# Kernel optimization log

Hardware: AMD Instinct MI355X
Metric: run time of the kernel (lower is better)

The kernel has to match this reference:

```python
import jax, jax.numpy as jnp
import numpy as np

N_NODES = 50000
N_EDGES = 800000
N_RELS = 65
D = 64
N_GRAPHS = 512


def setup_inputs() -> dict:
    key = jax.random.key(0)
    ks = jax.random.split(key, 20)
    inp = {
        "node_feats": jax.random.normal(ks[0], (N_NODES, D), dtype=jnp.float32),
        "etypes": jax.random.randint(ks[1], (N_EDGES,), 0, N_RELS),
        "src": jax.random.randint(ks[2], (N_EDGES,), 0, N_NODES),
        "dst": jax.random.randint(ks[3], (N_EDGES,), 0, N_NODES),
        "graph_ids": jnp.sort(jax.random.randint(ks[4], (N_NODES,), 0, N_GRAPHS)),
    }
    s = 1.0 / np.sqrt(D)
    # 3 RGCN layers: per-relation weights (basis with num_bases=num_rels == full) + bias
    for i, k in zip(range(1, 4), (ks[5], ks[6], ks[7])):
        inp[f"W_rel{i}"] = jax.random.normal(k, (N_RELS, D, D), dtype=jnp.float32) * s
        inp[f"b{i}"] = jnp.zeros((D,), dtype=jnp.float32)
    # 3 FC layers
    for i, k in zip(range(1, 4), (ks[8], ks[9], ks[10])):
        inp[f"fc_W{i}"] = jax.random.normal(k, (D, D), dtype=jnp.float32) * s
        inp[f"fc_b{i}"] = jnp.zeros((D,), dtype=jnp.float32)
    inp["pred_W"] = jax.random.normal(ks[11], (D, 2), dtype=jnp.float32) * s
    inp["pred_b"] = jnp.zeros((2,), dtype=jnp.float32)
    return inp


def _rgcn_layer(h, W, b, etypes, src, dst):
    # all-relation projection: [N, R, K]
    proj = jnp.einsum('nd,rdk->nrk', h, W)
    # per-edge gather of relation-specific message: [E, K]
    msg = proj[src, etypes]
    # scatter-sum into destination nodes
    agg = jax.ops.segment_sum(msg, dst, num_segments=h.shape[0])
    return jax.nn.relu(agg + b)


def reference(node_feats, etypes, src, dst, graph_ids,
              W_rel1, b1, W_rel2, b2, W_rel3, b3,
              fc_W1, fc_b1, fc_W2, fc_b2, fc_W3, fc_b3,
              pred_W, pred_b):
    h = node_feats
    h = _rgcn_layer(h, W_rel1, b1, etypes, src, dst)
    h = _rgcn_layer(h, W_rel2, b2, etypes, src, dst)
    h = _rgcn_layer(h, W_rel3, b3, etypes, src, dst)
    # sum-pool nodes per graph: [G, D]
    g = jax.ops.segment_sum(h, graph_ids, num_segments=N_GRAPHS)
    g = jax.nn.relu(g @ fc_W1 + fc_b1)
    g = jax.nn.relu(g @ fc_W2 + fc_b2)
    g = jax.nn.relu(g @ fc_W3 + fc_b3)
    return g @ pred_W + pred_b
```

## Files before the change

kernel.cpp:

```cpp
#include <hip/hip_runtime.h>
#include <hip/hip_bf16.h>

#define N_NODES 50000
#define N_EDGES 800000
#define N_RELS 65
#define DIM 64
#define N_GRAPHS 512

#define SORT_BLOCKS 256
#define CHUNK ((N_EDGES + SORT_BLOCKS - 1) / SORT_BLOCKS)

#define SCAN_BLK 512
#define NSCAN_BLKS ((N_NODES + SCAN_BLK - 1) / SCAN_BLK)

#define MSG_BLOCKS 1024
#define NWAVES (MSG_BLOCKS * 4)

typedef __attribute__((ext_vector_type(8))) short short8;
typedef __attribute__((ext_vector_type(4))) float f32x4;


__global__ void conv_h_zero_kernel(const float* __restrict__ x, __hip_bfloat16* __restrict__ y,
                                   int* __restrict__ cnt_d, int* __restrict__ cnt_g) {
    int i = blockIdx.x * 256 + threadIdx.x;
    if (i < N_NODES * DIM) y[i] = __float2bfloat16(x[i]);
    if (i < N_NODES) cnt_d[i] = 0;
    if (i < N_GRAPHS) cnt_g[i] = 0;
}

__global__ void conv_wt3_kernel(const float* __restrict__ W1, const float* __restrict__ W2,
                                const float* __restrict__ W3,
                                __hip_bfloat16* __restrict__ Wt1,
                                __hip_bfloat16* __restrict__ Wt2,
                                __hip_bfloat16* __restrict__ Wt3) {
    const int n = N_RELS * DIM * DIM;
    int i = blockIdx.x * 256 + threadIdx.x;
    if (i >= 3 * n) return;
    int which = i / n, j = i - which * n;
    const float* W = (which == 0) ? W1 : (which == 1) ? W2 : W3;
    __hip_bfloat16* Wt = (which == 0) ? Wt1 : (which == 1) ? Wt2 : Wt3;
    int r = j >> 12, rest = j & 4095;
    int nn = rest >> 6, k = rest & 63;
    Wt[(size_t)r * 4096 + nn * 64 + k] = __float2bfloat16(W[(size_t)r * 4096 + k * 64 + nn]);
}


__global__ __launch_bounds__(256) void hist2_kernel(const int* __restrict__ et,
                                                    int* __restrict__ blk_hist) {
    __shared__ int lh[N_RELS];
    int t = threadIdx.x, b = blockIdx.x;
    if (t < N_RELS) lh[t] = 0;
    __syncthreads();
    int lo = b * CHUNK;
    int hi = lo + CHUNK; if (hi > N_EDGES) hi = N_EDGES;
    for (int i = lo + t; i < hi; i += 256) atomicAdd(&lh[et[i]], 1);
    __syncthreads();
    if (t < N_RELS) blk_hist[b * N_RELS + t] = lh[t];
}

__global__ __launch_bounds__(256) void relwave_kernel(const int* __restrict__ blk_hist,
                                                      int* __restrict__ blk_off,
                                                      int* __restrict__ rel_tot) {
    int wave = blockIdx.x * 4 + (threadIdx.x >> 6);
    int lane = threadIdx.x & 63;
    if (wave >= N_RELS) return;
    int run = 0;
    for (int c = 0; c < SORT_BLOCKS; c += 64) {
        int b = c + lane;
        int v = blk_hist[b * N_RELS + wave];
        int x = v;
        #pragma unroll
        for (int off = 1; off < 64; off <<= 1) {
            int y = __shfl_up(x, off);
            if (lane >= off) x += y;
        }
        blk_off[b * N_RELS + wave] = run + x - v;
        run += __shfl(x, 63);
    }
    if (lane == 0) rel_tot[wave] = run;
}

__global__ __launch_bounds__(128) void relbase_kernel(const int* __restrict__ rel_tot,
                                                      int* __restrict__ rel_ptr,
                                                      int* __restrict__ tile_base) {
    __shared__ int tot[N_RELS];
    int t = threadIdx.x;
    if (t < N_RELS) tot[t] = rel_tot[t];
    __syncthreads();
    if (t == 0) {
        int s = 0, tt = 0;
        for (int q = 0; q < N_RELS; ++q) {
            rel_ptr[q] = s; s += tot[q];
            tile_base[q] = tt; tt += (tot[q] + 15) >> 4;
        }
        rel_ptr[N_RELS] = N_EDGES;
        tile_base[N_RELS] = tt;
    }
}

__global__ __launch_bounds__(256) void scatter2_kernel(
    const int* __restrict__ et, const int* __restrict__ src,
    const int* __restrict__ dst, const int* __restrict__ blk_off,
    const int* __restrict__ rel_ptr,
    int* __restrict__ src_s, int* __restrict__ dst_s) {
    __shared__ int cur[N_RELS];
    int t = threadIdx.x, b = blockIdx.x;
    if (t < N_RELS) cur[t] = blk_off[b * N_RELS + t] + rel_ptr[t];
    __syncthreads();
    int lo = b * CHUNK;
    int hi = lo + CHUNK; if (hi > N_EDGES) hi = N_EDGES;
    for (int i = lo + t; i < hi; i += 256) {
        int r = et[i];
        int p = atomicAdd(&cur[r], 1);
        src_s[p] = src[i];
        dst_s[p] = dst[i];
    }
}


__global__ void histdst_kernel(const int* __restrict__ dst, int* __restrict__ cnt_d) {
    int i = blockIdx.x * 256 + threadIdx.x;
    if (i < N_EDGES) atomicAdd(&cnt_d[dst[i]], 1);
}

__global__ __launch_bounds__(SCAN_BLK) void scanblk_kernel(const int* __restrict__ cnt,
                                                           int* __restrict__ outv,
                                                           int* __restrict__ blk_tot) {
    __shared__ int tmp[SCAN_BLK];
    int t = threadIdx.x;
    int i = blockIdx.x * SCAN_BLK + t;
    int v = (i < N_NODES) ? cnt[i] : 0;
    tmp[t] = v;
    __syncthreads();
    for (int off = 1; off < SCAN_BLK; off <<= 1) {
        int add = (t >= off) ? tmp[t - off] : 0;
        __syncthreads();
        tmp[t] += add;
        __syncthreads();
    }
    if (i < N_NODES) outv[i] = tmp[t] - v;
    if (t == SCAN_BLK - 1) blk_tot[blockIdx.x] = tmp[t];
}

__global__ void scantop_kernel(int* __restrict__ blk_tot, int* __restrict__ blk_base) {
    if (threadIdx.x == 0 && blockIdx.x == 0) {
        int run = 0;
        for (int b = 0; b < NSCAN_BLKS; ++b) { blk_base[b] = run; run += blk_tot[b]; }
    }
}

__global__ __launch_bounds__(SCAN_BLK) void scanadd_kernel(int* __restrict__ outv,
                                                           int* __restrict__ cursor,
                                                           const int* __restrict__ blk_base) {
    int i = blockIdx.x * SCAN_BLK + threadIdx.x;
    if (i < N_NODES) {
        int v = outv[i] + blk_base[blockIdx.x];
        outv[i] = v;
        cursor[i] = v;
    }
}

__global__ void dpos_kernel(const int* __restrict__ dst_s, int* __restrict__ cursor,
                            int* __restrict__ dpos) {
    int i = blockIdx.x * 256 + threadIdx.x;
    if (i < N_EDGES) dpos[i] = atomicAdd(&cursor[dst_s[i]], 1);
}


__global__ void histgid_kernel(const int* __restrict__ gid, int* __restrict__ cnt_g) {
    int i = blockIdx.x * 256 + threadIdx.x;
    if (i < N_NODES) atomicAdd(&cnt_g[gid[i]], 1);
}

__global__ __launch_bounds__(512) void scangid_kernel(const int* __restrict__ cnt_g,
                                                      int* __restrict__ g_ptr) {
    __shared__ int tmp[512];
    int t = threadIdx.x;
    int v = (t < N_GRAPHS) ? cnt_g[t] : 0;
    tmp[t] = v;
    __syncthreads();
    for (int off = 1; off < 512; off <<= 1) {
        int add = (t >= off) ? tmp[t - off] : 0;
        __syncthreads();
        tmp[t] += add;
        __syncthreads();
    }
    if (t < N_GRAPHS) g_ptr[t] = tmp[t] - v;
}


__global__ __launch_bounds__(256) void msg_mfma_kernel(
    const __hip_bfloat16* __restrict__ hb, const __hip_bfloat16* __restrict__ Wt,
    const int* __restrict__ rel_ptr, const int* __restrict__ tile_base,
    const int* __restrict__ src_s, const int* __restrict__ dpos,
    __hip_bfloat16* __restrict__ msg) {
    __shared__ __align__(16) unsigned short stA[4][16 * 72];
    __shared__ __align__(16) float stC[4][16 * 68];

    int t = threadIdx.x;
    int w = t >> 6, lane = t & 63;
    int quad = lane >> 4, m16 = lane & 15;
    int wave = blockIdx.x * 4 + w;

    int ntiles = tile_base[N_RELS];
    int tpw = (ntiles + NWAVES - 1) / NWAVES;
    int T = wave * tpw;
    int T1 = T + tpw; if (T1 > ntiles) T1 = ntiles;
    if (T >= T1) return;

    unsigned short* sa = &stA[w][0];
    float* sc = &stC[w][0];

    int r = 0;
    while (T >= tile_base[r + 1]) ++r;

    while (T < T1) {
        int chunk_end = tile_base[r + 1]; if (chunk_end > T1) chunk_end = T1;
        int e_base = rel_ptr[r], t_base = tile_base[r];
        int seg_end = rel_ptr[r + 1];

        const __hip_bfloat16* Wr = Wt + (size_t)r * (DIM * DIM);
        short8 bf00 = *(const short8*)(Wr + (0 * 16 + m16) * DIM + 0 * 32 + quad * 8);
        short8 bf01 = *(const short8*)(Wr + (1 * 16 + m16) * DIM + 0 * 32 + quad * 8);
        short8 bf02 = *(const short8*)(Wr + (2 * 16 + m16) * DIM + 0 * 32 + quad * 8);
        short8 bf03 = *(const short8*)(Wr + (3 * 16 + m16) * DIM + 0 * 32 + quad * 8);
        short8 bf10 = *(const short8*)(Wr + (0 * 16 + m16) * DIM + 1 * 32 + quad * 8);
        short8 bf11 = *(const short8*)(Wr + (1 * 16 + m16) * DIM + 1 * 32 + quad * 8);
        short8 bf12 = *(const short8*)(Wr + (2 * 16 + m16) * DIM + 1 * 32 + quad * 8);
        short8 bf13 = *(const short8*)(Wr + (3 * 16 + m16) * DIM + 1 * 32 + quad * 8);

        auto eidx = [&](int TT) {
            int i = e_base + (TT - t_base) * 16 + lane;
            return i < N_EDGES ? i : N_EDGES - 1;
        };

        int sv_c, dp_c, sv_n = 0, dp_n = 0, sv_nn = 0, dp_nn = 0;
        uint4 g0_c, g1_c;
        {
            int i0 = eidx(T);
            sv_c = src_s[i0]; dp_c = dpos[i0];
            int r0 = lane >> 3;
            int s0 = __shfl(sv_c, r0);
            int s1 = __shfl(sv_c, r0 + 8);
            g0_c = *(const uint4*)(hb + (size_t)s0 * DIM + (lane & 7) * 8);
            g1_c = *(const uint4*)(hb + (size_t)s1 * DIM + (lane & 7) * 8);
            if (T + 1 < chunk_end) {
                int i1 = eidx(T + 1);
                sv_n = src_s[i1]; dp_n = dpos[i1];
            }
        }

        for (; T < chunk_end; ++T) {
            int e0 = e_base + (T - t_base) * 16;
            int rows = seg_end - e0; if (rows > 16) rows = 16;

            int r0 = lane >> 3;
            *(uint4*)&sa[r0 * 72 + (lane & 7) * 8] = g0_c;
            *(uint4*)&sa[(r0 + 8) * 72 + (lane & 7) * 8] = g1_c;

            uint4 g0_n, g1_n;
            bool hasN = (T + 1 < chunk_end);
            if (hasN) {
                int s0 = __shfl(sv_n, r0);
                int s1 = __shfl(sv_n, r0 + 8);
                g0_n = *(const uint4*)(hb + (size_t)s0 * DIM + (lane & 7) * 8);
                g1_n = *(const uint4*)(hb + (size_t)s1 * DIM + (lane & 7) * 8);
            }
            if (T + 2 < chunk_end) {
                int i2 = eidx(T + 2);
                sv_nn = src_s[i2]; dp_nn = dpos[i2];
            }

            short8 a0 = *(const short8*)&sa[m16 * 72 + quad * 8];
            short8 a1 = *(const short8*)&sa[m16 * 72 + 32 + quad * 8];

            f32x4 c0 = {0.f, 0.f, 0.f, 0.f}, c1 = c0, c2 = c0, c3 = c0;
            c0 = __builtin_amdgcn_mfma_f32_16x16x32_bf16(a0, bf00, c0, 0, 0, 0);
            c1 = __builtin_amdgcn_mfma_f32_16x16x32_bf16(a0, bf01, c1, 0, 0, 0);
            c2 = __builtin_amdgcn_mfma_f32_16x16x32_bf16(a0, bf02, c2, 0, 0, 0);
            c3 = __builtin_amdgcn_mfma_f32_16x16x32_bf16(a0, bf03, c3, 0, 0, 0);
            c0 = __builtin_amdgcn_mfma_f32_16x16x32_bf16(a1, bf10, c0, 0, 0, 0);
            c1 = __builtin_amdgcn_mfma_f32_16x16x32_bf16(a1, bf11, c1, 0, 0, 0);
            c2 = __builtin_amdgcn_mfma_f32_16x16x32_bf16(a1, bf12, c2, 0, 0, 0);
            c3 = __builtin_amdgcn_mfma_f32_16x16x32_bf16(a1, bf13, c3, 0, 0, 0);

            #pragma unroll
            for (int reg = 0; reg < 4; ++reg) {
                int rr = (quad * 4 + reg) * 68 + m16;
                sc[rr +  0] = c0[reg];
                sc[rr + 16] = c1[reg];
                sc[rr + 32] = c2[reg];
                sc[rr + 48] = c3[reg];
            }

            int orow = lane >> 2;
            if (orow < rows) {
                int c0i = (lane & 3) * 16;
                float vs[16];
                *(f32x4*)&vs[0]  = *(const f32x4*)&sc[orow * 68 + c0i + 0];
                *(f32x4*)&vs[4]  = *(const f32x4*)&sc[orow * 68 + c0i + 4];
                *(f32x4*)&vs[8]  = *(const f32x4*)&sc[orow * 68 + c0i + 8];
                *(f32x4*)&vs[12] = *(const f32x4*)&sc[orow * 68 + c0i + 12];
                unsigned short us[16];
                #pragma unroll
                for (int i = 0; i < 16; ++i)
                    us[i] = __hip_bfloat16_raw(__float2bfloat16(vs[i])).x;
                int dprow = __shfl(dp_c, orow);
                __hip_bfloat16* dst = msg + (size_t)dprow * DIM + c0i;
                *(uint4*)dst = *(const uint4*)&us[0];
                *(uint4*)(dst + 8) = *(const uint4*)&us[8];
            }

            if (hasN) { g0_c = g0_n; g1_c = g1_n; }
            sv_c = sv_n; dp_c = dp_n;
            sv_n = sv_nn; dp_n = dp_nn;
        }
        ++r;
        while (T < T1 && T >= tile_base[r + 1]) ++r;
    }
}


__global__ __launch_bounds__(256) void agg_kernel(
    const __hip_bfloat16* __restrict__ msg, const int* __restrict__ row_ptr,
    const int* __restrict__ cnt_d, const float* __restrict__ b,
    __hip_bfloat16* __restrict__ hout) {
    int wave = blockIdx.x * 4 + (threadIdx.x >> 6);
    int lane = threadIdx.x & 63;
    if (wave >= N_NODES) return;
    int j0 = row_ptr[wave];
    int n  = cnt_d[wave];
    int rgrp = lane >> 3, dgrp = lane & 7;

    float a[8] = {0.f, 0.f, 0.f, 0.f, 0.f, 0.f, 0.f, 0.f};
    for (int jj = 0; jj < n; jj += 8) {
        int row = jj + rgrp;
        if (row < n) {
            uint4 d = *(const uint4*)(msg + (size_t)(j0 + row) * DIM + dgrp * 8);
            a[0] += __uint_as_float(d.x << 16);
            a[1] += __uint_as_float(d.x & 0xffff0000u);
            a[2] += __uint_as_float(d.y << 16);
            a[3] += __uint_as_float(d.y & 0xffff0000u);
            a[4] += __uint_as_float(d.z << 16);
            a[5] += __uint_as_float(d.z & 0xffff0000u);
            a[6] += __uint_as_float(d.w << 16);
            a[7] += __uint_as_float(d.w & 0xffff0000u);
        }
    }
    #pragma unroll
    for (int i = 0; i < 8; ++i) {
        a[i] += __shfl_xor(a[i], 8);
        a[i] += __shfl_xor(a[i], 16);
        a[i] += __shfl_xor(a[i], 32);
    }
    if (rgrp == 0) {
        unsigned short us[8];
        #pragma unroll
        for (int i = 0; i < 8; ++i) {
            float v = a[i] + b[dgrp * 8 + i];
            us[i] = __hip_bfloat16_raw(__float2bfloat16(v > 0.f ? v : 0.f)).x;
        }
        *(uint4*)(hout + (size_t)wave * DIM + dgrp * 8) = *(const uint4*)us;
    }
}


__global__ __launch_bounds__(256) void poolfc_kernel(
    const __hip_bfloat16* __restrict__ h, const int* __restrict__ g_ptr,
    const int* __restrict__ cnt_g,
    const float* __restrict__ W1, const float* __restrict__ b1,
    const float* __restrict__ W2, const float* __restrict__ b2,
    const float* __restrict__ W3, const float* __restrict__ b3,
    const float* __restrict__ pW, const float* __restrict__ pb,
    float* __restrict__ out) {
    int wave = blockIdx.x * 4 + (threadIdx.x >> 6);
    int lane = threadIdx.x & 63;
    if (wave >= N_GRAPHS) return;
    int j0 = g_ptr[wave];
    int n  = cnt_g[wave];
    int rgrp = lane >> 3, dgrp = lane & 7;

    float a[8] = {0.f, 0.f, 0.f, 0.f, 0.f, 0.f, 0.f, 0.f};
    for (int jj = 0; jj < n; jj += 8) {
        int row = jj + rgrp;
        if (row < n) {
            uint4 d = *(const uint4*)(h + (size_t)(j0 + row) * DIM + dgrp * 8);
            a[0] += __uint_as_float(d.x << 16);
            a[1] += __uint_as_float(d.x & 0xffff0000u);
            a[2] += __uint_as_float(d.y << 16);
            a[3] += __uint_as_float(d.y & 0xffff0000u);
            a[4] += __uint_as_float(d.z << 16);
            a[5] += __uint_as_float(d.z & 0xffff0000u);
            a[6] += __uint_as_float(d.w << 16);
            a[7] += __uint_as_float(d.w & 0xffff0000u);
        }
    }
    #pragma unroll
    for (int i = 0; i < 8; ++i) {
        a[i] += __shfl_xor(a[i], 8);
        a[i] += __shfl_xor(a[i], 16);
        a[i] += __shfl_xor(a[i], 32);
    }
    float v;
    {
        float acc = b1[lane];
        #pragma unroll
        for (int o = 0; o < 8; ++o)
            #pragma unroll
            for (int q = 0; q < 8; ++q)
                acc += __shfl(a[o], q) * W1[(q * 8 + o) * DIM + lane];
        v = acc > 0.f ? acc : 0.f;
    }
    {
        float acc = b2[lane];
        #pragma unroll
        for (int d = 0; d < DIM; ++d)
            acc += __shfl(v, d) * W2[d * DIM + lane];
        v = acc > 0.f ? acc : 0.f;
    }
    {
        float acc = b3[lane];
        #pragma unroll
        for (int d = 0; d < DIM; ++d)
            acc += __shfl(v, d) * W3[d * DIM + lane];
        v = acc > 0.f ? acc : 0.f;
    }
    float p0 = v * pW[lane * 2 + 0];
    float p1 = v * pW[lane * 2 + 1];
    #pragma unroll
    for (int off = 32; off > 0; off >>= 1) {
        p0 += __shfl_down(p0, off);
        p1 += __shfl_down(p1, off);
    }
    if (lane == 0) {
        out[wave * 2 + 0] = p0 + pb[0];
        out[wave * 2 + 1] = p1 + pb[1];
    }
}


extern "C" void kernel_launch(void* const* d_in, const int* in_sizes, int n_in,
                              void* d_out, int out_size, void* d_ws, size_t ws_size,
                              hipStream_t stream) {
    const float* node_feats = (const float*)d_in[0];
    const int*   etypes     = (const int*)d_in[1];
    const int*   src        = (const int*)d_in[2];
    const int*   dst        = (const int*)d_in[3];
    const int*   graph_ids  = (const int*)d_in[4];
    const float* W1 = (const float*)d_in[5];
    const float* b1 = (const float*)d_in[6];
    const float* W2 = (const float*)d_in[7];
    const float* b2 = (const float*)d_in[8];
    const float* W3 = (const float*)d_in[9];
    const float* b3 = (const float*)d_in[10];
    const float* fcW1 = (const float*)d_in[11];
    const float* fcb1 = (const float*)d_in[12];
    const float* fcW2 = (const float*)d_in[13];
    const float* fcb2 = (const float*)d_in[14];
    const float* fcW3 = (const float*)d_in[15];
    const float* fcb3 = (const float*)d_in[16];
    const float* pW = (const float*)d_in[17];
    const float* pb = (const float*)d_in[18];
    float* out = (float*)d_out;

    char* p = (char*)d_ws;
    auto alloc = [&](size_t bytes) -> void* {
        void* r = (void*)p;
        p += (bytes + 255) & ~(size_t)255;
        return r;
    };
    int* blk_hist  = (int*)alloc((size_t)SORT_BLOCKS * N_RELS * sizeof(int));
    int* blk_off   = (int*)alloc((size_t)SORT_BLOCKS * N_RELS * sizeof(int));
    int* rel_tot   = (int*)alloc(N_RELS * sizeof(int));
    int* rel_ptr   = (int*)alloc((N_RELS + 1) * sizeof(int));
    int* tile_base = (int*)alloc((N_RELS + 1) * sizeof(int));
    int* src_s     = (int*)alloc((size_t)N_EDGES * sizeof(int));
    int* dst_s     = (int*)alloc((size_t)N_EDGES * sizeof(int));
    int* dpos      = (int*)alloc((size_t)N_EDGES * sizeof(int));
    int* cnt_d     = (int*)alloc((size_t)N_NODES * sizeof(int));
    int* row_ptr   = (int*)alloc((size_t)N_NODES * sizeof(int));
    int* cursor_d  = (int*)alloc((size_t)N_NODES * sizeof(int));
    int* blk_tot   = (int*)alloc(NSCAN_BLKS * sizeof(int));
    int* blk_base  = (int*)alloc(NSCAN_BLKS * sizeof(int));
    int* cnt_g     = (int*)alloc(N_GRAPHS * sizeof(int));
    int* g_ptr     = (int*)alloc(N_GRAPHS * sizeof(int));
    __hip_bfloat16* hb0 = (__hip_bfloat16*)alloc((size_t)N_NODES * DIM * sizeof(__hip_bfloat16));
    __hip_bfloat16* hb1 = (__hip_bfloat16*)alloc((size_t)N_NODES * DIM * sizeof(__hip_bfloat16));
    __hip_bfloat16* Wt1 = (__hip_bfloat16*)alloc((size_t)N_RELS * DIM * DIM * sizeof(__hip_bfloat16));
    __hip_bfloat16* Wt2 = (__hip_bfloat16*)alloc((size_t)N_RELS * DIM * DIM * sizeof(__hip_bfloat16));
    __hip_bfloat16* Wt3 = (__hip_bfloat16*)alloc((size_t)N_RELS * DIM * DIM * sizeof(__hip_bfloat16));
    __hip_bfloat16* msg = (__hip_bfloat16*)alloc((size_t)N_EDGES * DIM * sizeof(__hip_bfloat16));

    const int EBLK = (N_EDGES + 255) / 256;
    const int HBLK = (N_NODES * DIM + 255) / 256;
    const int W3BLK = (3 * N_RELS * DIM * DIM + 255) / 256;
    const int NBLK256 = (N_NODES + 255) / 256;
    const int AGG_BLOCKS = (N_NODES + 3) / 4;

    conv_h_zero_kernel<<<HBLK, 256, 0, stream>>>(node_feats, hb0, cnt_d, cnt_g);
    conv_wt3_kernel<<<W3BLK, 256, 0, stream>>>(W1, W2, W3, Wt1, Wt2, Wt3);

    hist2_kernel<<<SORT_BLOCKS, 256, 0, stream>>>(etypes, blk_hist);
    relwave_kernel<<<(N_RELS + 3) / 4, 256, 0, stream>>>(blk_hist, blk_off, rel_tot);
    relbase_kernel<<<1, 128, 0, stream>>>(rel_tot, rel_ptr, tile_base);
    scatter2_kernel<<<SORT_BLOCKS, 256, 0, stream>>>(etypes, src, dst, blk_off, rel_ptr,
                                                     src_s, dst_s);

    histdst_kernel<<<EBLK, 256, 0, stream>>>(dst, cnt_d);
    scanblk_kernel<<<NSCAN_BLKS, SCAN_BLK, 0, stream>>>(cnt_d, row_ptr, blk_tot);
    scantop_kernel<<<1, 64, 0, stream>>>(blk_tot, blk_base);
    scanadd_kernel<<<NSCAN_BLKS, SCAN_BLK, 0, stream>>>(row_ptr, cursor_d, blk_base);
    dpos_kernel<<<EBLK, 256, 0, stream>>>(dst_s, cursor_d, dpos);

    histgid_kernel<<<NBLK256, 256, 0, stream>>>(graph_ids, cnt_g);
    scangid_kernel<<<1, 512, 0, stream>>>(cnt_g, g_ptr);

    msg_mfma_kernel<<<MSG_BLOCKS, 256, 0, stream>>>(hb0, Wt1, rel_ptr, tile_base,
                                                    src_s, dpos, msg);
    agg_kernel<<<AGG_BLOCKS, 256, 0, stream>>>(msg, row_ptr, cnt_d, b1, hb1);

    msg_mfma_kernel<<<MSG_BLOCKS, 256, 0, stream>>>(hb1, Wt2, rel_ptr, tile_base,
                                                    src_s, dpos, msg);
    agg_kernel<<<AGG_BLOCKS, 256, 0, stream>>>(msg, row_ptr, cnt_d, b2, hb0);

    msg_mfma_kernel<<<MSG_BLOCKS, 256, 0, stream>>>(hb0, Wt3, rel_ptr, tile_base,
                                                    src_s, dpos, msg);
    agg_kernel<<<AGG_BLOCKS, 256, 0, stream>>>(msg, row_ptr, cnt_d, b3, hb1);

    poolfc_kernel<<<(N_GRAPHS + 3) / 4, 256, 0, stream>>>(hb1, g_ptr, cnt_g,
                                                          fcW1, fcb1, fcW2, fcb2,
                                                          fcW3, fcb3, pW, pb, out);
}
```

Baseline: 421.4 us.

## Merge preprocessing kernels and deepen gather prefetch in message kernel

Folds the weight transpose, destination histogram and graph-id histogram into the relation histogram kernel. Merges the relation scan with the base computation, and the graph-id scan with the top-level scan, which cuts the launch count by about five. The message MFMA kernel now prefetches edge indices three tiles ahead and gathers two tiles ahead to hide gather latency. This raises register pressure, and the merged histogram kernel runs its loops serially over only 256 blocks, so it has less parallelism than the separate launches.

```diff
diff --git a/kernel.cpp b/kernel.cpp
--- a/kernel.cpp
+++ b/kernel.cpp
@@ -28,64 +28,66 @@
     if (i < N_GRAPHS) cnt_g[i] = 0;
 }
 
-__global__ void conv_wt3_kernel(const float* __restrict__ W1, const float* __restrict__ W2,
-                                const float* __restrict__ W3,
-                                __hip_bfloat16* __restrict__ Wt1,
-                                __hip_bfloat16* __restrict__ Wt2,
-                                __hip_bfloat16* __restrict__ Wt3) {
-    const int n = N_RELS * DIM * DIM;
-    int i = blockIdx.x * 256 + threadIdx.x;
-    if (i >= 3 * n) return;
-    int which = i / n, j = i - which * n;
-    const float* W = (which == 0) ? W1 : (which == 1) ? W2 : W3;
-    __hip_bfloat16* Wt = (which == 0) ? Wt1 : (which == 1) ? Wt2 : Wt3;
-    int r = j >> 12, rest = j & 4095;
-    int nn = rest >> 6, k = rest & 63;
-    Wt[(size_t)r * 4096 + nn * 64 + k] = __float2bfloat16(W[(size_t)r * 4096 + k * 64 + nn]);
-}
-
-
-__global__ __launch_bounds__(256) void hist2_kernel(const int* __restrict__ et,
-                                                    int* __restrict__ blk_hist) {
+
+__global__ __launch_bounds__(256) void hist_all_kernel(
+    const int* __restrict__ et, const int* __restrict__ dst,
+    const int* __restrict__ gid, int* __restrict__ blk_hist,
+    int* __restrict__ cnt_d, int* __restrict__ cnt_g,
+    const float* __restrict__ W1, const float* __restrict__ W2,
+    const float* __restrict__ W3,
+    __hip_bfloat16* __restrict__ Wt1, __hip_bfloat16* __restrict__ Wt2,
+    __hip_bfloat16* __restrict__ Wt3) {
     __shared__ int lh[N_RELS];
     int t = threadIdx.x, b = blockIdx.x;
+    int gtid = b * 256 + t;
     if (t < N_RELS) lh[t] = 0;
     __syncthreads();
     int lo = b * CHUNK;
     int hi = lo + CHUNK; if (hi > N_EDGES) hi = N_EDGES;
-    for (int i = lo + t; i < hi; i += 256) atomicAdd(&lh[et[i]], 1);
+    for (int i = lo + t; i < hi; i += 256) {
+        atomicAdd(&lh[et[i]], 1);
+        atomicAdd(&cnt_d[dst[i]], 1);
+    }
+    for (int i = gtid; i < N_NODES; i += SORT_BLOCKS * 256)
+        atomicAdd(&cnt_g[gid[i]], 1);
+    const int WN = N_RELS * DIM * DIM;
+    for (int i = gtid; i < 3 * WN; i += SORT_BLOCKS * 256) {
+        int which = i / WN, j = i - which * WN;
+        const float* W = (which == 0) ? W1 : (which == 1) ? W2 : W3;
+        __hip_bfloat16* Wt = (which == 0) ? Wt1 : (which == 1) ? Wt2 : Wt3;
+        int r = j >> 12, rest = j & 4095;
+        int nn = rest >> 6, k = rest & 63;
+        Wt[(size_t)r * 4096 + nn * 64 + k] =
+            __float2bfloat16(W[(size_t)r * 4096 + k * 64 + nn]);
+    }
     __syncthreads();
     if (t < N_RELS) blk_hist[b * N_RELS + t] = lh[t];
 }
 
-__global__ __launch_bounds__(256) void relwave_kernel(const int* __restrict__ blk_hist,
-                                                      int* __restrict__ blk_off,
-                                                      int* __restrict__ rel_tot) {
-    int wave = blockIdx.x * 4 + (threadIdx.x >> 6);
-    int lane = threadIdx.x & 63;
-    if (wave >= N_RELS) return;
-    int run = 0;
-    for (int c = 0; c < SORT_BLOCKS; c += 64) {
-        int b = c + lane;
-        int v = blk_hist[b * N_RELS + wave];
-        int x = v;
-        #pragma unroll
-        for (int off = 1; off < 64; off <<= 1) {
-            int y = __shfl_up(x, off);
-            if (lane >= off) x += y;
-        }
-        blk_off[b * N_RELS + wave] = run + x - v;
-        run += __shfl(x, 63);
-    }
-    if (lane == 0) rel_tot[wave] = run;
-}
-
-__global__ __launch_bounds__(128) void relbase_kernel(const int* __restrict__ rel_tot,
-                                                      int* __restrict__ rel_ptr,
-                                                      int* __restrict__ tile_base) {
+
+__global__ __launch_bounds__(1024) void relwave2_kernel(const int* __restrict__ blk_hist,
+                                                        int* __restrict__ blk_off,
+                                                        int* __restrict__ rel_ptr,
+                                                        int* __restrict__ tile_base) {
     __shared__ int tot[N_RELS];
     int t = threadIdx.x;
-    if (t < N_RELS) tot[t] = rel_tot[t];
+    int w = t >> 6, lane = t & 63;
+    for (int r = w; r < N_RELS; r += 16) {
+        int run = 0;
+        for (int c = 0; c < SORT_BLOCKS; c += 64) {
+            int b = c + lane;
+            int v = blk_hist[b * N_RELS + r];
+            int x = v;
+            #pragma unroll
+            for (int off = 1; off < 64; off <<= 1) {
+                int y = __shfl_up(x, off);
+                if (lane >= off) x += y;
+            }
+            blk_off[b * N_RELS + r] = run + x - v;
+            run += __shfl(x, 63);
+        }
+        if (lane == 0) tot[r] = run;
+    }
     __syncthreads();
     if (t == 0) {
         int s = 0, tt = 0;
@@ -97,6 +99,7 @@
         tile_base[N_RELS] = tt;
     }
 }
+
 
 __global__ __launch_bounds__(256) void scatter2_kernel(
     const int* __restrict__ et, const int* __restrict__ src,
@@ -118,11 +121,6 @@
 }
 
 
-__global__ void histdst_kernel(const int* __restrict__ dst, int* __restrict__ cnt_d) {
-    int i = blockIdx.x * 256 + threadIdx.x;
-    if (i < N_EDGES) atomicAdd(&cnt_d[dst[i]], 1);
-}
-
 __global__ __launch_bounds__(SCAN_BLK) void scanblk_kernel(const int* __restrict__ cnt,
                                                            int* __restrict__ outv,
                                                            int* __restrict__ blk_tot) {
@@ -142,10 +140,28 @@
     if (t == SCAN_BLK - 1) blk_tot[blockIdx.x] = tmp[t];
 }
 
-__global__ void scantop_kernel(int* __restrict__ blk_tot, int* __restrict__ blk_base) {
-    if (threadIdx.x == 0 && blockIdx.x == 0) {
+__global__ __launch_bounds__(64) void scantop_gid_kernel(
+    const int* __restrict__ blk_tot, int* __restrict__ blk_base,
+    const int* __restrict__ cnt_g, int* __restrict__ g_ptr) {
+    int lane = threadIdx.x;
+    if (blockIdx.x == 0) {
+        if (lane == 0) {
+            int run = 0;
+            for (int b = 0; b < NSCAN_BLKS; ++b) { blk_base[b] = run; run += blk_tot[b]; }
+        }
+    } else {
         int run = 0;
-        for (int b = 0; b < NSCAN_BLKS; ++b) { blk_base[b] = run; run += blk_tot[b]; }
+        for (int c = 0; c < N_GRAPHS; c += 64) {
+            int v = cnt_g[c + lane];
+            int x = v;
+            #pragma unroll
+            for (int off = 1; off < 64; off <<= 1) {
+                int y = __shfl_up(x, off);
+                if (lane >= off) x += y;
+            }
+            g_ptr[c + lane] = run + x - v;
+            run += __shfl(x, 63);
+        }
     }
 }
 
@@ -167,28 +183,6 @@
 }
 
 
-__global__ void histgid_kernel(const int* __restrict__ gid, int* __restrict__ cnt_g) {
-    int i = blockIdx.x * 256 + threadIdx.x;
-    if (i < N_NODES) atomicAdd(&cnt_g[gid[i]], 1);
-}
-
-__global__ __launch_bounds__(512) void scangid_kernel(const int* __restrict__ cnt_g,
-                                                      int* __restrict__ g_ptr) {
-    __shared__ int tmp[512];
-    int t = threadIdx.x;
-    int v = (t < N_GRAPHS) ? cnt_g[t] : 0;
-    tmp[t] = v;
-    __syncthreads();
-    for (int off = 1; off < 512; off <<= 1) {
-        int add = (t >= off) ? tmp[t - off] : 0;
-        __syncthreads();
-        tmp[t] += add;
-        __syncthreads();
-    }
-    if (t < N_GRAPHS) g_ptr[t] = tmp[t] - v;
-}
-
-
 __global__ __launch_bounds__(256) void msg_mfma_kernel(
     const __hip_bfloat16* __restrict__ hb, const __hip_bfloat16* __restrict__ Wt,
     const int* __restrict__ rel_ptr, const int* __restrict__ tile_base,
@@ -210,6 +204,7 @@
 
     unsigned short* sa = &stA[w][0];
     float* sc = &stC[w][0];
+    int r0l = lane >> 3;
 
     int r = 0;
     while (T >= tile_base[r + 1]) ++r;
@@ -220,56 +215,46 @@
         int seg_end = rel_ptr[r + 1];
 
         const __hip_bfloat16* Wr = Wt + (size_t)r * (DIM * DIM);
-        short8 bf00 = *(const short8*)(Wr + (0 * 16 + m16) * DIM + 0 * 32 + quad * 8);
-        short8 bf01 = *(const short8*)(Wr + (1 * 16 + m16) * DIM + 0 * 32 + quad * 8);
-        short8 bf02 = *(const short8*)(Wr + (2 * 16 + m16) * DIM + 0 * 32 + quad * 8);
-        short8 bf03 = *(const short8*)(Wr + (3 * 16 + m16) * DIM + 0 * 32 + quad * 8);
-        short8 bf10 = *(const short8*)(Wr + (0 * 16 + m16) * DIM + 1 * 32 + quad * 8);
-        short8 bf11 = *(const short8*)(Wr + (1 * 16 + m16) * DIM + 1 * 32 + quad * 8);
-        short8 bf12 = *(const short8*)(Wr + (2 * 16 + m16) * DIM + 1 * 32 + quad * 8);
-        short8 bf13 = *(const short8*)(Wr + (3 * 16 + m16) * DIM + 1 * 32 + quad * 8);
-
-        auto eidx = [&](int TT) {
-            int i = e_base + (TT - t_base) * 16 + lane;
-            return i < N_EDGES ? i : N_EDGES - 1;
+        short8 bf00 = *(const short8*)(Wr + (0 * 16 + m16) * DIM + quad * 8);
+        short8 bf01 = *(const short8*)(Wr + (1 * 16 + m16) * DIM + quad * 8);
+        short8 bf02 = *(const short8*)(Wr + (2 * 16 + m16) * DIM + quad * 8);
+        short8 bf03 = *(const short8*)(Wr + (3 * 16 + m16) * DIM + quad * 8);
+        short8 bf10 = *(const short8*)(Wr + (0 * 16 + m16) * DIM + 32 + quad * 8);
+        short8 bf11 = *(const short8*)(Wr + (1 * 16 + m16) * DIM + 32 + quad * 8);
+        short8 bf12 = *(const short8*)(Wr + (2 * 16 + m16) * DIM + 32 + quad * 8);
+        short8 bf13 = *(const short8*)(Wr + (3 * 16 + m16) * DIM + 32 + quad * 8);
+
+        auto loadidx = [&](int TT, int& sv, int& dp) {
+            int TC = TT < chunk_end ? TT : chunk_end - 1;
+            int i = e_base + (TC - t_base) * 16 + lane;
+            if (i >= N_EDGES) i = N_EDGES - 1;
+            sv = src_s[i]; dp = dpos[i];
         };
-
-        int sv_c, dp_c, sv_n = 0, dp_n = 0, sv_nn = 0, dp_nn = 0;
-        uint4 g0_c, g1_c;
-        {
-            int i0 = eidx(T);
-            sv_c = src_s[i0]; dp_c = dpos[i0];
-            int r0 = lane >> 3;
-            int s0 = __shfl(sv_c, r0);
-            int s1 = __shfl(sv_c, r0 + 8);
-            g0_c = *(const uint4*)(hb + (size_t)s0 * DIM + (lane & 7) * 8);
-            g1_c = *(const uint4*)(hb + (size_t)s1 * DIM + (lane & 7) * 8);
-            if (T + 1 < chunk_end) {
-                int i1 = eidx(T + 1);
-                sv_n = src_s[i1]; dp_n = dpos[i1];
-            }
-        }
+        auto gather = [&](int sv, uint4& g0, uint4& g1) {
+            int s0 = __shfl(sv, r0l);
+            int s1 = __shfl(sv, r0l + 8);
+            g0 = *(const uint4*)(hb + (size_t)s0 * DIM + (lane & 7) * 8);
+            g1 = *(const uint4*)(hb + (size_t)s1 * DIM + (lane & 7) * 8);
+        };
+
+        int sv0, dp0, sv1, dp1, sv2, dp2, sv3, dp3;
+        uint4 gc0, gc1, gn0, gn1;
+        loadidx(T,     sv0, dp0);
+        loadidx(T + 1, sv1, dp1);
+        loadidx(T + 2, sv2, dp2);
+        gather(sv0, gc0, gc1);
+        gather(sv1, gn0, gn1);
 
         for (; T < chunk_end; ++T) {
             int e0 = e_base + (T - t_base) * 16;
             int rows = seg_end - e0; if (rows > 16) rows = 16;
 
-            int r0 = lane >> 3;
-            *(uint4*)&sa[r0 * 72 + (lane & 7) * 8] = g0_c;
-            *(uint4*)&sa[(r0 + 8) * 72 + (lane & 7) * 8] = g1_c;
-
-            uint4 g0_n, g1_n;
-            bool hasN = (T + 1 < chunk_end);
-            if (hasN) {
-                int s0 = __shfl(sv_n, r0);
-                int s1 = __shfl(sv_n, r0 + 8);
-                g0_n = *(const uint4*)(hb + (size_t)s0 * DIM + (lane & 7) * 8);
-                g1_n = *(const uint4*)(hb + (size_t)s1 * DIM + (lane & 7) * 8);
-            }
-            if (T + 2 < chunk_end) {
-                int i2 = eidx(T + 2);
-                sv_nn = src_s[i2]; dp_nn = dpos[i2];
-            }
+            uint4 gnn0, gnn1;
+            gather(sv2, gnn0, gnn1);
+            loadidx(T + 3, sv3, dp3);
+
+            *(uint4*)&sa[r0l * 72 + (lane & 7) * 8] = gc0;
+            *(uint4*)&sa[(r0l + 8) * 72 + (lane & 7) * 8] = gc1;
 
             short8 a0 = *(const short8*)&sa[m16 * 72 + quad * 8];
             short8 a1 = *(const short8*)&sa[m16 * 72 + 32 + quad * 8];
@@ -305,15 +290,14 @@
                 #pragma unroll
                 for (int i = 0; i < 16; ++i)
                     us[i] = __hip_bfloat16_raw(__float2bfloat16(vs[i])).x;
-                int dprow = __shfl(dp_c, orow);
-                __hip_bfloat16* dst = msg + (size_t)dprow * DIM + c0i;
-                *(uint4*)dst = *(const uint4*)&us[0];
-                *(uint4*)(dst + 8) = *(const uint4*)&us[8];
+                int dprow = __shfl(dp0, orow);
+                __hip_bfloat16* dstp = msg + (size_t)dprow * DIM + c0i;
+                *(uint4*)dstp = *(const uint4*)&us[0];
+                *(uint4*)(dstp + 8) = *(const uint4*)&us[8];
             }
 
-            if (hasN) { g0_c = g0_n; g1_c = g1_n; }
-            sv_c = sv_n; dp_c = dp_n;
-            sv_n = sv_nn; dp_n = dp_nn;
+            gc0 = gn0; gc1 = gn1; gn0 = gnn0; gn1 = gnn1;
+            sv0 = sv1; dp0 = dp1; sv1 = sv2; dp1 = dp2; sv2 = sv3; dp2 = dp3;
         }
         ++r;
         while (T < T1 && T >= tile_base[r + 1]) ++r;
@@ -471,7 +455,6 @@
     };
     int* blk_hist  = (int*)alloc((size_t)SORT_BLOCKS * N_RELS * sizeof(int));
     int* blk_off   = (int*)alloc((size_t)SORT_BLOCKS * N_RELS * sizeof(int));
-    int* rel_tot   = (int*)alloc(N_RELS * sizeof(int));
     int* rel_ptr   = (int*)alloc((N_RELS + 1) * sizeof(int));
     int* tile_base = (int*)alloc((N_RELS + 1) * sizeof(int));
     int* src_s     = (int*)alloc((size_t)N_EDGES * sizeof(int));
@@ -493,27 +476,19 @@
 
     const int EBLK = (N_EDGES + 255) / 256;
     const int HBLK = (N_NODES * DIM + 255) / 256;
-    const int W3BLK = (3 * N_RELS * DIM * DIM + 255) / 256;
-    const int NBLK256 = (N_NODES + 255) / 256;
     const int AGG_BLOCKS = (N_NODES + 3) / 4;
 
     conv_h_zero_kernel<<<HBLK, 256, 0, stream>>>(node_feats, hb0, cnt_d, cnt_g);
-    conv_wt3_kernel<<<W3BLK, 256, 0, stream>>>(W1, W2, W3, Wt1, Wt2, Wt3);
-
-    hist2_kernel<<<SORT_BLOCKS, 256, 0, stream>>>(etypes, blk_hist);
-    relwave_kernel<<<(N_RELS + 3) / 4, 256, 0, stream>>>(blk_hist, blk_off, rel_tot);
-    relbase_kernel<<<1, 128, 0, stream>>>(rel_tot, rel_ptr, tile_base);
+    hist_all_kernel<<<SORT_BLOCKS, 256, 0, stream>>>(etypes, dst, graph_ids, blk_hist,
+                                                     cnt_d, cnt_g, W1, W2, W3,
+                                                     Wt1, Wt2, Wt3);
+    relwave2_kernel<<<1, 1024, 0, stream>>>(blk_hist, blk_off, rel_ptr, tile_base);
     scatter2_kernel<<<SORT_BLOCKS, 256, 0, stream>>>(etypes, src, dst, blk_off, rel_ptr,
                                                      src_s, dst_s);
-
-    histdst_kernel<<<EBLK, 256, 0, stream>>>(dst, cnt_d);
     scanblk_kernel<<<NSCAN_BLKS, SCAN_BLK, 0, stream>>>(cnt_d, row_ptr, blk_tot);
-    scantop_kernel<<<1, 64, 0, stream>>>(blk_tot, blk_base);
+    scantop_gid_kernel<<<2, 64, 0, stream>>>(blk_tot, blk_base, cnt_g, g_ptr);
     scanadd_kernel<<<NSCAN_BLKS, SCAN_BLK, 0, stream>>>(row_ptr, cursor_d, blk_base);
     dpos_kernel<<<EBLK, 256, 0, stream>>>(dst_s, cursor_d, dpos);
-
-    histgid_kernel<<<NBLK256, 256, 0, stream>>>(graph_ids, cnt_g);
-    scangid_kernel<<<1, 512, 0, stream>>>(cnt_g, g_ptr);
 
     msg_mfma_kernel<<<MSG_BLOCKS, 256, 0, stream>>>(hb0, Wt1, rel_ptr, tile_base,
                                                     src_s, dpos, msg);
```

Measured after the change: 424.1 us. No clear change (+0.6%).
